# Optimization experiments

Hardware: AMD Instinct MI355X
Metric: run time of the kernel (lower is better)

## Reference

```python
import jax, jax.numpy as jnp
import numpy as np

D_MSA = 256
D_PAIR = 128
N_HEADS = 8
HEAD_DIM = D_MSA // N_HEADS
EPS = 1e-5


def setup_inputs() -> dict:
    key = jax.random.key(0)
    ks = jax.random.split(key, 14)
    s = 0.02
    return {
        "msa": jax.random.normal(ks[0], (1, 64, 256, D_MSA), dtype=jnp.float32),
        "pair": jax.random.normal(ks[1], (1, 256, 256, D_PAIR), dtype=jnp.float32),
        "Wq": jax.random.normal(ks[2], (D_MSA, D_MSA), dtype=jnp.float32) * s,
        "bq": jnp.zeros((D_MSA,), jnp.float32),
        "Wk": jax.random.normal(ks[3], (D_MSA, D_MSA), dtype=jnp.float32) * s,
        "bk": jnp.zeros((D_MSA,), jnp.float32),
        "Wv": jax.random.normal(ks[4], (D_MSA, D_MSA), dtype=jnp.float32) * s,
        "bv": jnp.zeros((D_MSA,), jnp.float32),
        "Wpb": jax.random.normal(ks[5], (D_PAIR, N_HEADS), dtype=jnp.float32) * s,
        "bpb": jnp.zeros((N_HEADS,), jnp.float32),
        "Wo": jax.random.normal(ks[6], (D_MSA, D_MSA), dtype=jnp.float32) * s,
        "bo": jnp.zeros((D_MSA,), jnp.float32),
        "gamma": jnp.ones((D_MSA,), jnp.float32),
        "beta": jnp.zeros((D_MSA,), jnp.float32),
    }


def reference(msa, pair, Wq, bq, Wk, bk, Wv, bv, Wpb, bpb, Wo, bo, gamma, beta):
    B, N, L, D = msa.shape
    H, Hd = N_HEADS, HEAD_DIM
    # projections -> (B, N, L, H, Hd)
    q = (msa @ Wq + bq).reshape(B, N, L, H, Hd)
    k = (msa @ Wk + bk).reshape(B, N, L, H, Hd)
    v = (msa @ Wv + bv).reshape(B, N, L, H, Hd)
    # scores: (B, N, H, L, L)
    scores = jnp.einsum('bnihd,bnjhd->bnhij', q, k) / jnp.sqrt(jnp.float32(Hd))
    # pair bias: (B, L, L, H) -> (B, H, L, L), broadcast over N
    pb = jnp.transpose(pair @ Wpb + bpb, (0, 3, 1, 2))
    scores = scores + pb[:, None]
    attn = jax.nn.softmax(scores, axis=-1)
    attn_out = jnp.einsum('bnhij,bnjhd->bnihd', attn, v).reshape(B, N, L, D)
    attn_out = attn_out @ Wo + bo
    # residual + LayerNorm
    x = msa + attn_out
    mu = jnp.mean(x, axis=-1, keepdims=True)
    var = jnp.var(x, axis=-1, keepdims=True)
    return (x - mu) * jax.lax.rsqrt(var + EPS) * gamma + beta
```

## Files before the change

### kernel.cpp

```cpp
#include <hip/hip_runtime.h>

#define NSEQ 64
#define LL   256
#define DD   256
#define HH   8
#define HDIM 32

typedef short short8  __attribute__((ext_vector_type(8)));
typedef short short4v __attribute__((ext_vector_type(4)));
typedef float float4v __attribute__((ext_vector_type(4)));

#define MFMA16(a,b,c) __builtin_amdgcn_mfma_f32_16x16x32_bf16((a),(b),(c),0,0,0)

__device__ __forceinline__ float4v zero4() {
  float4v z;
  z[0] = 0.f; z[1] = 0.f; z[2] = 0.f; z[3] = 0.f;
  return z;
}

__device__ __forceinline__ short f2b(float f) {
  unsigned u = __float_as_uint(f);
  u = (u + 0x7fffu + ((u >> 16) & 1u)) >> 16;
  return (short)u;
}

__device__ __forceinline__ float b2f(short s) {
  return __uint_as_float(((unsigned)(unsigned short)s) << 16);
}

__device__ __forceinline__ short8 cvt8(const float* p) {
  float4 a = *(const float4*)p;
  float4 b = *(const float4*)(p + 4);
  short8 r;
  r[0] = f2b(a.x); r[1] = f2b(a.y); r[2] = f2b(a.z); r[3] = f2b(a.w);
  r[4] = f2b(b.x); r[5] = f2b(b.y); r[6] = f2b(b.z); r[7] = f2b(b.w);
  return r;
}

__device__ __forceinline__ void ld_lds16(const void* g, void* l) {
  __builtin_amdgcn_global_load_lds(
      (const __attribute__((address_space(1))) unsigned int*)g,
      (__attribute__((address_space(3))) unsigned int*)l, 16, 0, 0);
}
#define WAIT_VM0() __builtin_amdgcn_s_waitcnt(0x0F70)

#define WT_OFF    0
#define PB_OFF    (4*65536*2)
#define PBF_OFF   (PB_OFF + 8*65536*2)
#define Q_OFF     (PB_OFF + 8*65536*4)
#define K_OFF     (Q_OFF  + 16384*256*2)
#define VT_OFF    (K_OFF  + 16384*256*2)
#define MSA16_OFF (VT_OFF + 16384*256*2)
#define O_OFF     MSA16_OFF

__global__ __launch_bounds__(256) void k1_prep(
    const float* __restrict__ msa,  const float* __restrict__ pair,
    const float* __restrict__ Wq,   const float* __restrict__ Wk,
    const float* __restrict__ Wv,   const float* __restrict__ Wpb,
    const float* __restrict__ bpb,  const float* __restrict__ Wo,
    char* __restrict__ ws)
{
  __shared__ short lds[32 * 264];
  int bx = blockIdx.x, tid = threadIdx.x;
  if (bx < 1024) {
    short* pb16 = (short*)(ws + PB_OFF);
    for (int i = tid; i < 16 * 136; i += 256) lds[i] = 0;
    __syncthreads();
    {
      float4 wv4 = *(const float4*)&Wpb[tid * 4];
      int kk = (tid * 4) >> 3, n0 = (tid * 4) & 7;
      lds[(n0 + 0) * 136 + kk] = f2b(wv4.x);
      lds[(n0 + 1) * 136 + kk] = f2b(wv4.y);
      lds[(n0 + 2) * 136 + kk] = f2b(wv4.z);
      lds[(n0 + 3) * 136 + kk] = f2b(wv4.w);
    }
    __syncthreads();
    int w = tid >> 6, l = tid & 63, q = l >> 4, c = l & 15;
    int base = bx * 64 + w * 16;
    short8 bf[4], af[4];
#pragma unroll
    for (int ks = 0; ks < 4; ks++)
      bf[ks] = *(const short8*)&lds[c * 136 + ks * 32 + q * 8];
#pragma unroll
    for (int ks = 0; ks < 4; ks++)
      af[ks] = cvt8(&pair[(base + c) * 128 + ks * 32 + q * 8]);
    float4v acc = zero4();
#pragma unroll
    for (int ks = 0; ks < 4; ks++) acc = MFMA16(af[ks], bf[ks], acc);
    if (c < 8) {
      float bias = bpb[c];
      short4v o;
#pragma unroll
      for (int r = 0; r < 4; r++) o[r] = f2b(acc[r] + bias);
      *(short4v*)&pb16[c * 65536 + base + q * 4] = o;
    }
  } else if (bx < 1536) {
    int b3 = bx - 1024;
    const float* src = msa + b3 * 8192;
    short* dst = (short*)(ws + MSA16_OFF) + b3 * 8192;
#pragma unroll
    for (int i = 0; i < 8; i++) {
      int idx = i * 1024 + tid * 4;
      float4 v = *(const float4*)&src[idx];
      short4v s;
      s[0] = f2b(v.x); s[1] = f2b(v.y); s[2] = f2b(v.z); s[3] = f2b(v.w);
      *(short4v*)&dst[idx] = s;
    }
  } else {
    int b2 = bx - 1536;
    int mat = b2 >> 3, kt = b2 & 7;
    const float* W = (mat == 0) ? Wq : (mat == 1) ? Wk : (mat == 2) ? Wv : Wo;
    short* wt = (short*)(ws + WT_OFF) + mat * 65536;
#pragma unroll
    for (int i = 0; i < 8; i++) {
      int idx = i * 1024 + tid * 4;
      int k = idx >> 8, n = idx & 255;
      float4 v = *(const float4*)&W[(kt * 32 + k) * 256 + n];
      short4v s;
      s[0] = f2b(v.x); s[1] = f2b(v.y); s[2] = f2b(v.z); s[3] = f2b(v.w);
      *(short4v*)&lds[k * 264 + n] = s;
    }
    __syncthreads();
    int n = tid;
#pragma unroll
    for (int g = 0; g < 4; g++) {
      short8 o;
#pragma unroll
      for (int j = 0; j < 8; j++) o[j] = lds[(g * 8 + j) * 264 + n];
      *(short8*)&wt[n * 256 + kt * 32 + g * 8] = o;
    }
  }
}

__global__ __launch_bounds__(256) void k2_qkv(
    const float* __restrict__ bq, const float* __restrict__ bk,
    const float* __restrict__ bv, char* __restrict__ ws)
{
  __shared__ __align__(16) short lsA[128 * 128];
  __shared__ __align__(16) short lsB[128 * 128];
  int bx = blockIdx.x, tid = threadIdx.x;
  if (bx >= 768) {
    int b = bx - 768;
    int it16 = b & 15;
    const short* src = (const short*)(ws + PB_OFF) + (b >> 4) * 65536 + it16 * 4096;
    short* pbf = (short*)(ws + PBF_OFF);
    short* lt = lsA;
#pragma unroll
    for (int i2 = 0; i2 < 2; i2++) {
      int idx = i2 * 2048 + tid * 8;
      *(short8*)&lt[(idx >> 8) * 264 + (idx & 255)] = *(const short8*)&src[idx];
    }
    __syncthreads();
#pragma unroll
    for (int i2 = 0; i2 < 4; i2++) {
      int fid = i2 * 256 + tid;
      int jt = fid >> 6, lane = fid & 63;
      int qp = lane >> 4, cp = lane & 15;
      short4v v;
#pragma unroll
      for (int r = 0; r < 4; r++)
        v[r] = lt[(qp * 4 + r) * 264 + jt * 16 + cp];
      *(short4v*)&pbf[((b * 16 + jt) * 64 + lane) * 4] = v;
    }
    return;
  }
  int rt = bx & 127, ct = bx >> 7;
  int m = ct >> 1, cb = (ct & 1) * 128;
  int R0 = rt * 128;
  const short* msa16 = (const short*)(ws + MSA16_OFF);
  const short* wt = (const short*)(ws + WT_OFF) + m * 65536;
  int w = tid >> 6, l = tid & 63, q = l >> 4, c = l & 15;
  int WR = (w & 1) * 64, WC = (w >> 1) * 64;
  float4v acc[4][4];
#pragma unroll
  for (int mt = 0; mt < 4; mt++)
#pragma unroll
    for (int nt = 0; nt < 4; nt++) acc[mt][nt] = zero4();

#pragma unroll 1
  for (int kk = 0; kk < 2; kk++) {
    if (kk) __syncthreads();
#pragma unroll
    for (int i = 0; i < 8; i++) {
      int ci = i * 256 + tid;
      int r = ci >> 4, pos = ci & 15;
      int kc = pos ^ (r & 7);
      ld_lds16(&msa16[(R0 + r) * 256 + kk * 128 + kc * 8], &lsA[ci * 8]);
    }
#pragma unroll
    for (int i = 0; i < 8; i++) {
      int ci = i * 256 + tid;
      int r = ci >> 4, pos = ci & 15;
      int kc = pos ^ (r & 7);
      ld_lds16(&wt[(cb + r) * 256 + kk * 128 + kc * 8], &lsB[ci * 8]);
    }
    WAIT_VM0();
    __syncthreads();
#pragma unroll
    for (int ks = 0; ks < 4; ks++) {
      short8 af[4], bf[4];
#pragma unroll
      for (int mt = 0; mt < 4; mt++) {
        int r = WR + mt * 16 + c;
        int phys = (ks * 4 + q) ^ (r & 7);
        af[mt] = *(const short8*)&lsA[r * 128 + phys * 8];
      }
#pragma unroll
      for (int nt = 0; nt < 4; nt++) {
        int r = WC + nt * 16 + c;
        int phys = (ks * 4 + q) ^ (r & 7);
        bf[nt] = *(const short8*)&lsB[r * 128 + phys * 8];
      }
#pragma unroll
      for (int mt = 0; mt < 4; mt++)
#pragma unroll
        for (int nt = 0; nt < 4; nt++)
          acc[mt][nt] = MFMA16(af[mt], bf[nt], acc[mt][nt]);
    }
  }

  const float* bp = (m == 0) ? bq : (m == 1) ? bk : bv;
  int n = R0 >> 8;
  if (m < 2) {
    short* dst = (short*)(ws + (m == 0 ? Q_OFF : K_OFF));
#pragma unroll
    for (int nt = 0; nt < 4; nt++) {
      int ch = cb + WC + nt * 16 + c;
      float bb = bp[ch];
      int h = ch >> 5, hd = ch & 31;
#pragma unroll
      for (int mt = 0; mt < 4; mt++) {
        int i0 = (R0 & 255) + WR + mt * 16 + q * 4;
#pragma unroll
        for (int r = 0; r < 4; r++)
          dst[((n * HH + h) * 256 + i0 + r) * HDIM + hd] = f2b(acc[mt][nt][r] + bb);
      }
    }
  } else {
    short* vt = (short*)(ws + VT_OFF);
#pragma unroll
    for (int nt = 0; nt < 4; nt++) {
      int ch = cb + WC + nt * 16 + c;
      float bb = bp[ch];
#pragma unroll
      for (int mt = 0; mt < 4; mt++) {
        int j0 = (R0 & 255) + WR + mt * 16 + q * 4;
        short4v s4;
#pragma unroll
        for (int r = 0; r < 4; r++) s4[r] = f2b(acc[mt][nt][r] + bb);
        *(short4v*)&vt[((n * HH + (ch >> 5)) * HDIM + (ch & 31)) * 256 + j0] = s4;
      }
    }
  }
}

__global__ __launch_bounds__(256) void k3_attn(char* __restrict__ ws)
{
  __shared__ short P[64 * 264];
  int bx = blockIdx.x, tid = threadIdx.x;
  int qq = bx >> 9, grp = bx & 511;
  int n = grp >> 3, h = grp & 7;
  int w = tid >> 6, l = tid & 63, q = l >> 4, c = l & 15;
  const short* qh = (const short*)(ws + Q_OFF) + (n * HH + h) * 256 * HDIM;
  const short* kh = (const short*)(ws + K_OFF) + (n * HH + h) * 256 * HDIM;
  const short* vt = (const short*)(ws + VT_OFF) + (n * HH + h) * HDIM * 256;
  const short* pbf = (const short*)(ws + PBF_OFF) + (h * 16 + qq * 4 + w) * 16 * 256;
  short* os = (short*)(ws + O_OFF);
  const float scale = 0.17677669529663687f;
  int i0 = qq * 64 + w * 16;
  short8 aq = *(const short8*)&qh[(i0 + c) * HDIM + q * 8];
  float4v s[16];
#pragma unroll
  for (int jt = 0; jt < 16; jt++) {
    short8 bk8 = *(const short8*)&kh[(jt * 16 + c) * HDIM + q * 8];
    s[jt] = MFMA16(aq, bk8, zero4());
  }
#pragma unroll
  for (int jt = 0; jt < 16; jt++) {
    short4v pv = *(const short4v*)&pbf[(jt * 64 + l) * 4];
#pragma unroll
    for (int r = 0; r < 4; r++)
      s[jt][r] = __builtin_fmaf(s[jt][r], scale, b2f(pv[r]));
  }
  float inv[4];
#pragma unroll
  for (int r = 0; r < 4; r++) {
    float m = s[0][r];
#pragma unroll
    for (int jt = 1; jt < 16; jt++) m = fmaxf(m, s[jt][r]);
    m = fmaxf(m, __shfl_xor(m, 1, 64));
    m = fmaxf(m, __shfl_xor(m, 2, 64));
    m = fmaxf(m, __shfl_xor(m, 4, 64));
    m = fmaxf(m, __shfl_xor(m, 8, 64));
    float rs = 0.f;
#pragma unroll
    for (int jt = 0; jt < 16; jt++) {
      float p = __expf(s[jt][r] - m);
      s[jt][r] = p;
      rs += p;
    }
    rs += __shfl_xor(rs, 1, 64);
    rs += __shfl_xor(rs, 2, 64);
    rs += __shfl_xor(rs, 4, 64);
    rs += __shfl_xor(rs, 8, 64);
    inv[r] = 1.f / rs;
  }
#pragma unroll
  for (int jt = 0; jt < 16; jt++)
#pragma unroll
    for (int r = 0; r < 4; r++)
      P[(w * 16 + q * 4 + r) * 264 + jt * 16 + c] = f2b(s[jt][r]);
  float4v o0 = zero4(), o1 = zero4();
#pragma unroll
  for (int kk = 0; kk < 8; kk++) {
    short8 ap = *(const short8*)&P[(w * 16 + c) * 264 + kk * 32 + q * 8];
    short8 b0 = *(const short8*)&vt[c * 256 + kk * 32 + q * 8];
    short8 b1 = *(const short8*)&vt[(16 + c) * 256 + kk * 32 + q * 8];
    o0 = MFMA16(ap, b0, o0);
    o1 = MFMA16(ap, b1, o1);
  }
#pragma unroll
  for (int r = 0; r < 4; r++) {
    os[(n * 256 + i0 + q * 4 + r) * 256 + h * 32 + c]      = f2b(o0[r] * inv[r]);
    os[(n * 256 + i0 + q * 4 + r) * 256 + h * 32 + 16 + c] = f2b(o1[r] * inv[r]);
  }
}

__global__ __launch_bounds__(256) void k4_out(
    const float* __restrict__ msa, const float* __restrict__ bo,
    const float* __restrict__ gamma, const float* __restrict__ beta,
    const char* __restrict__ ws, float* __restrict__ out)
{
  __shared__ float lnbuf[2][4][16];
  int bx = blockIdx.x, tid = threadIdx.x;
  int w = tid >> 6, l = tid & 63, q = l >> 4, c = l & 15;
  int R0 = bx * 16;
  const short* osrc = (const short*)(ws + O_OFF);
  const short* wto  = (const short*)(ws + WT_OFF) + 3 * 65536;
  short8 af[8];
#pragma unroll
  for (int ks = 0; ks < 8; ks++)
    af[ks] = *(const short8*)&osrc[(R0 + c) * 256 + ks * 32 + q * 8];
  float4v acc[4];
#pragma unroll
  for (int nt = 0; nt < 4; nt++) acc[nt] = zero4();
#pragma unroll
  for (int ks = 0; ks < 8; ks++) {
#pragma unroll
    for (int nt = 0; nt < 4; nt++) {
      short8 bf = *(const short8*)&wto[(w * 64 + nt * 16 + c) * 256 + ks * 32 + q * 8];
      acc[nt] = MFMA16(af[ks], bf, acc[nt]);
    }
  }
  float s1[4] = {0, 0, 0, 0}, s2[4] = {0, 0, 0, 0};
#pragma unroll
  for (int nt = 0; nt < 4; nt++) {
    int col = w * 64 + nt * 16 + c;
    float bb = bo[col];
#pragma unroll
    for (int r = 0; r < 4; r++) {
      float x = acc[nt][r] + bb + msa[(R0 + q * 4 + r) * 256 + col];
      acc[nt][r] = x;
      s1[r] += x;
      s2[r] = __builtin_fmaf(x, x, s2[r]);
    }
  }
#pragma unroll
  for (int r = 0; r < 4; r++) {
    float a = s1[r], b = s2[r];
    a += __shfl_xor(a, 1, 64); b += __shfl_xor(b, 1, 64);
    a += __shfl_xor(a, 2, 64); b += __shfl_xor(b, 2, 64);
    a += __shfl_xor(a, 4, 64); b += __shfl_xor(b, 4, 64);
    a += __shfl_xor(a, 8, 64); b += __shfl_xor(b, 8, 64);
    if (c == 0) {
      lnbuf[0][w][q * 4 + r] = a;
      lnbuf[1][w][q * 4 + r] = b;
    }
  }
  __syncthreads();
  float mu[4], rsd[4];
#pragma unroll
  for (int r = 0; r < 4; r++) {
    int row = q * 4 + r;
    float a = lnbuf[0][0][row] + lnbuf[0][1][row] + lnbuf[0][2][row] + lnbuf[0][3][row];
    float b = lnbuf[1][0][row] + lnbuf[1][1][row] + lnbuf[1][2][row] + lnbuf[1][3][row];
    float m = a * (1.f / 256.f);
    float v = __builtin_fmaf(-m, m, b * (1.f / 256.f));
    mu[r] = m;
    rsd[r] = rsqrtf(v + 1e-5f);
  }
#pragma unroll
  for (int nt = 0; nt < 4; nt++) {
    int col = w * 64 + nt * 16 + c;
    float g = gamma[col], bt = beta[col];
#pragma unroll
    for (int r = 0; r < 4; r++)
      out[(R0 + q * 4 + r) * 256 + col] =
          (acc[nt][r] - mu[r]) * rsd[r] * g + bt;
  }
}

extern "C" void kernel_launch(void* const* d_in, const int* in_sizes, int n_in,
                              void* d_out, int out_size, void* d_ws, size_t ws_size,
                              hipStream_t stream)
{
  const float* msa   = (const float*)d_in[0];
  const float* pair  = (const float*)d_in[1];
  const float* Wq    = (const float*)d_in[2];
  const float* bq    = (const float*)d_in[3];
  const float* Wk    = (const float*)d_in[4];
  const float* bk    = (const float*)d_in[5];
  const float* Wv    = (const float*)d_in[6];
  const float* bv    = (const float*)d_in[7];
  const float* Wpb   = (const float*)d_in[8];
  const float* bpb   = (const float*)d_in[9];
  const float* Wo    = (const float*)d_in[10];
  const float* bo    = (const float*)d_in[11];
  const float* gamma = (const float*)d_in[12];
  const float* beta  = (const float*)d_in[13];
  char* ws = (char*)d_ws;
  float* out = (float*)d_out;

  hipLaunchKernelGGL(k1_prep, dim3(1568), dim3(256), 0, stream,
                     msa, pair, Wq, Wk, Wv, Wpb, bpb, Wo, ws);
  hipLaunchKernelGGL(k2_qkv, dim3(896), dim3(256), 0, stream,
                     bq, bk, bv, ws);
  hipLaunchKernelGGL(k3_attn, dim3(2048), dim3(256), 0, stream, ws);
  hipLaunchKernelGGL(k4_out, dim3(1024), dim3(256), 0, stream,
                     msa, bo, gamma, beta, ws, out);
}
```

Baseline: 182.0 us.

## Write pair bias in fragment layout directly and stream softmax without max

```diff
diff --git a/kernel.cpp b/kernel.cpp
--- a/kernel.cpp
+++ b/kernel.cpp
@@ -63,7 +63,6 @@
   __shared__ short lds[32 * 264];
   int bx = blockIdx.x, tid = threadIdx.x;
   if (bx < 1024) {
-    short* pb16 = (short*)(ws + PB_OFF);
     for (int i = tid; i < 16 * 136; i += 256) lds[i] = 0;
     __syncthreads();
     {
@@ -89,10 +88,13 @@
     for (int ks = 0; ks < 4; ks++) acc = MFMA16(af[ks], bf[ks], acc);
     if (c < 8) {
       float bias = bpb[c];
-      short4v o;
-#pragma unroll
-      for (int r = 0; r < 4; r++) o[r] = f2b(acc[r] + bias);
-      *(short4v*)&pb16[c * 65536 + base + q * 4] = o;
+      int i = bx >> 2, it = i >> 4, lr = i & 15;
+      int jt = (bx & 3) * 4 + w;
+      short* pbf = (short*)(ws + PBF_OFF);
+      int b0 = c * 65536 + it * 4096 + jt * 256 + (lr >> 2) * 64 + (lr & 3) + q * 16;
+#pragma unroll
+      for (int r = 0; r < 4; r++)
+        pbf[b0 + r * 4] = f2b(acc[r] + bias);
     }
   } else if (bx < 1536) {
     int b3 = bx - 1024;
@@ -139,31 +141,6 @@
   __shared__ __align__(16) short lsA[128 * 128];
   __shared__ __align__(16) short lsB[128 * 128];
   int bx = blockIdx.x, tid = threadIdx.x;
-  if (bx >= 768) {
-    int b = bx - 768;
-    int it16 = b & 15;
-    const short* src = (const short*)(ws + PB_OFF) + (b >> 4) * 65536 + it16 * 4096;
-    short* pbf = (short*)(ws + PBF_OFF);
-    short* lt = lsA;
-#pragma unroll
-    for (int i2 = 0; i2 < 2; i2++) {
-      int idx = i2 * 2048 + tid * 8;
-      *(short8*)&lt[(idx >> 8) * 264 + (idx & 255)] = *(const short8*)&src[idx];
-    }
-    __syncthreads();
-#pragma unroll
-    for (int i2 = 0; i2 < 4; i2++) {
-      int fid = i2 * 256 + tid;
-      int jt = fid >> 6, lane = fid & 63;
-      int qp = lane >> 4, cp = lane & 15;
-      short4v v;
-#pragma unroll
-      for (int r = 0; r < 4; r++)
-        v[r] = lt[(qp * 4 + r) * 264 + jt * 16 + cp];
-      *(short4v*)&pbf[((b * 16 + jt) * 64 + lane) * 4] = v;
-    }
-    return;
-  }
   int rt = bx & 127, ct = bx >> 7;
   int m = ct >> 1, cb = (ct & 1) * 128;
   int R0 = rt * 128;
@@ -256,7 +233,7 @@
 
 __global__ __launch_bounds__(256) void k3_attn(char* __restrict__ ws)
 {
-  __shared__ short P[64 * 264];
+  __shared__ short P[4][16 * 136];
   int bx = blockIdx.x, tid = threadIdx.x;
   int qq = bx >> 9, grp = bx & 511;
   int n = grp >> 3, h = grp & 7;
@@ -264,60 +241,56 @@
   const short* qh = (const short*)(ws + Q_OFF) + (n * HH + h) * 256 * HDIM;
   const short* kh = (const short*)(ws + K_OFF) + (n * HH + h) * 256 * HDIM;
   const short* vt = (const short*)(ws + VT_OFF) + (n * HH + h) * HDIM * 256;
-  const short* pbf = (const short*)(ws + PBF_OFF) + (h * 16 + qq * 4 + w) * 16 * 256;
+  const short* pbf = (const short*)(ws + PBF_OFF) + (h * 16 + qq * 4 + w) * 4096;
   short* os = (short*)(ws + O_OFF);
+  short* Pw = &P[w][0];
   const float scale = 0.17677669529663687f;
   int i0 = qq * 64 + w * 16;
   short8 aq = *(const short8*)&qh[(i0 + c) * HDIM + q * 8];
-  float4v s[16];
-#pragma unroll
-  for (int jt = 0; jt < 16; jt++) {
-    short8 bk8 = *(const short8*)&kh[(jt * 16 + c) * HDIM + q * 8];
-    s[jt] = MFMA16(aq, bk8, zero4());
-  }
-#pragma unroll
-  for (int jt = 0; jt < 16; jt++) {
-    short4v pv = *(const short4v*)&pbf[(jt * 64 + l) * 4];
-#pragma unroll
-    for (int r = 0; r < 4; r++)
-      s[jt][r] = __builtin_fmaf(s[jt][r], scale, b2f(pv[r]));
+  float4v o0 = zero4(), o1 = zero4();
+  float rs[4] = {0.f, 0.f, 0.f, 0.f};
+  float4v s[8];
+#pragma unroll 1
+  for (int half = 0; half < 2; half++) {
+    int jb = half * 8;
+#pragma unroll
+    for (int jt = 0; jt < 8; jt++) {
+      short8 bk8 = *(const short8*)&kh[((jb + jt) * 16 + c) * HDIM + q * 8];
+      s[jt] = MFMA16(aq, bk8, zero4());
+    }
+#pragma unroll
+    for (int jt = 0; jt < 8; jt++) {
+      short4v pv = *(const short4v*)&pbf[((jb + jt) * 64 + l) * 4];
+#pragma unroll
+      for (int r = 0; r < 4; r++) {
+        float p = __expf(__builtin_fmaf(s[jt][r], scale, b2f(pv[r])));
+        s[jt][r] = p;
+        rs[r] += p;
+      }
+    }
+#pragma unroll
+    for (int jt = 0; jt < 8; jt++)
+#pragma unroll
+      for (int r = 0; r < 4; r++)
+        Pw[(q * 4 + r) * 136 + jt * 16 + c] = f2b(s[jt][r]);
+#pragma unroll
+    for (int kk = 0; kk < 4; kk++) {
+      short8 ap = *(const short8*)&Pw[c * 136 + kk * 32 + q * 8];
+      short8 b0 = *(const short8*)&vt[c * 256 + (jb + kk * 2) * 16 + q * 8];
+      short8 b1 = *(const short8*)&vt[(16 + c) * 256 + (jb + kk * 2) * 16 + q * 8];
+      o0 = MFMA16(ap, b0, o0);
+      o1 = MFMA16(ap, b1, o1);
+    }
   }
   float inv[4];
 #pragma unroll
   for (int r = 0; r < 4; r++) {
-    float m = s[0][r];
-#pragma unroll
-    for (int jt = 1; jt < 16; jt++) m = fmaxf(m, s[jt][r]);
-    m = fmaxf(m, __shfl_xor(m, 1, 64));
-    m = fmaxf(m, __shfl_xor(m, 2, 64));
-    m = fmaxf(m, __shfl_xor(m, 4, 64));
-    m = fmaxf(m, __shfl_xor(m, 8, 64));
-    float rs = 0.f;
-#pragma unroll
-    for (int jt = 0; jt < 16; jt++) {
-      float p = __expf(s[jt][r] - m);
-      s[jt][r] = p;
-      rs += p;
-    }
-    rs += __shfl_xor(rs, 1, 64);
-    rs += __shfl_xor(rs, 2, 64);
-    rs += __shfl_xor(rs, 4, 64);
-    rs += __shfl_xor(rs, 8, 64);
-    inv[r] = 1.f / rs;
-  }
-#pragma unroll
-  for (int jt = 0; jt < 16; jt++)
-#pragma unroll
-    for (int r = 0; r < 4; r++)
-      P[(w * 16 + q * 4 + r) * 264 + jt * 16 + c] = f2b(s[jt][r]);
-  float4v o0 = zero4(), o1 = zero4();
-#pragma unroll
-  for (int kk = 0; kk < 8; kk++) {
-    short8 ap = *(const short8*)&P[(w * 16 + c) * 264 + kk * 32 + q * 8];
-    short8 b0 = *(const short8*)&vt[c * 256 + kk * 32 + q * 8];
-    short8 b1 = *(const short8*)&vt[(16 + c) * 256 + kk * 32 + q * 8];
-    o0 = MFMA16(ap, b0, o0);
-    o1 = MFMA16(ap, b1, o1);
+    float a = rs[r];
+    a += __shfl_xor(a, 1, 64);
+    a += __shfl_xor(a, 2, 64);
+    a += __shfl_xor(a, 4, 64);
+    a += __shfl_xor(a, 8, 64);
+    inv[r] = 1.f / a;
   }
 #pragma unroll
   for (int r = 0; r < 4; r++) {
@@ -423,7 +396,7 @@
 
   hipLaunchKernelGGL(k1_prep, dim3(1568), dim3(256), 0, stream,
                      msa, pair, Wq, Wk, Wv, Wpb, bpb, Wo, ws);
-  hipLaunchKernelGGL(k2_qkv, dim3(896), dim3(256), 0, stream,
+  hipLaunchKernelGGL(k2_qkv, dim3(768), dim3(256), 0, stream,
                      bq, bk, bv, ws);
   hipLaunchKernelGGL(k3_attn, dim3(2048), dim3(256), 0, stream, ws);
   hipLaunchKernelGGL(k4_out, dim3(1024), dim3(256), 0, stream,
```

Result: no change. 181.6 us (-0.2%).
